# Optimization experiments

Hardware: AMD Instinct MI355X
Metric: run time of the kernel (lower is better)

The kernel has to match this reference:

```python
import jax, jax.numpy as jnp
import numpy as np

B, T, C, H, N_LAYER, LAYER_ID = 4, 2048, 1024, 16, 12, 6
N = C // H
Q = 256  # T % 256 == 0 -> chunk size used by the module


def setup_inputs():
    key = jax.random.key(0)
    ks = jax.random.split(key, 9)
    r0 = LAYER_ID / (N_LAYER - 1)
    r1 = 1.0 - LAYER_ID / N_LAYER
    ddd = (jnp.arange(C, dtype=jnp.float32) / C)[None, None, :]
    h = jnp.arange(C, dtype=jnp.float32)
    s = 1.0 / np.sqrt(C)
    return {
        "x": jax.random.normal(ks[0], (B, T, C), jnp.float32),
        "time_maa_x": 1.0 - ddd ** r1,
        "time_maa_w": 1.0 - ddd ** r1,
        "time_maa_k": 1.0 - ddd ** r1,
        "time_maa_v": 1.0 - (ddd ** r1 + 0.3 * r0),
        "time_maa_r": 1.0 - ddd ** (0.5 * r1),
        "maa_w1": jax.random.uniform(ks[1], (C, 4 * 32), jnp.float32, minval=-0.01, maxval=0.01),
        "maa_w2": jax.random.uniform(ks[2], (4, 32, C), jnp.float32, minval=-0.01, maxval=0.01),
        "decay_w1": jax.random.uniform(ks[3], (C, 64), jnp.float32, minval=-0.01, maxval=0.01),
        "decay_w2": jax.random.uniform(ks[4], (64, C), jnp.float32, minval=-0.01, maxval=0.01),
        "time_decay": (-6.0 + 5.0 * (h / (C - 1)) ** (0.7 + 1.3 * r0))[None, None, :],
        "time_faaaa": (r0 * (1.0 - h / (C - 1))).reshape(1, H, 1, 1, N),
        "Wr": jax.random.normal(ks[5], (C, C), jnp.float32) * s,
        "Wk": jax.random.normal(ks[6], (C, C), jnp.float32) * s,
        "Wv": jax.random.normal(ks[7], (C, C), jnp.float32) * s,
        "Wo": jax.random.normal(ks[8], (C, C), jnp.float32) * s,
        "ln_g": jnp.ones((C,), jnp.float32),
        "ln_b": jnp.zeros((C,), jnp.float32),
    }


def _forward(x, time_maa_x, time_maa_w, time_maa_k, time_maa_v, time_maa_r,
             maa_w1, maa_w2, decay_w1, decay_w2, time_decay, time_faaaa,
             Wr, Wk, Wv, Wo, ln_g, ln_b):
    b, t, c = x.shape
    nc = t // Q
    # time_shift: zero-pad one step at front of time axis, drop last step
    xx = jnp.pad(x, ((0, 0), (1, 0), (0, 0)))[:, :-1] - x
    xxx = x + xx * time_maa_x
    m = jnp.tanh(xxx @ maa_w1).reshape(b, t, 4, -1)  # [B,T,4,32]
    m = jnp.einsum('btfd,fdc->fbtc', m, maa_w2)       # [4,B,T,C]
    mw, mk, mv, mr = m[0], m[1], m[2], m[3]
    xw = x + xx * (time_maa_w + mw)
    xk = x + xx * (time_maa_k + mk)
    xv = x + xx * (time_maa_v + mv)
    xr = x + xx * (time_maa_r + mr)
    r = (xr @ Wr).reshape(b, t, H, N).transpose(0, 2, 1, 3)  # [B,H,T,N]
    k = (xk @ Wk).reshape(b, t, H, N).transpose(0, 2, 1, 3)
    v = (xv @ Wv).reshape(b, t, H, N).transpose(0, 2, 1, 3)
    w = time_decay + jnp.tanh(xw @ decay_w1) @ decay_w2      # [B,T,C]
    w = w.reshape(b, t, H, N).transpose(0, 2, 1, 3).mean(axis=-1)  # [B,H,T]
    w_log = -jnp.exp(w)
    wc = w_log.reshape(b, H, nc, Q, 1)
    wc_cum = jnp.cumsum(wc, axis=-2)
    shifted = jnp.pad(wc_cum, ((0, 0), (0, 0), (0, 0), (1, 0), (0, 0)))[..., :-1, :]
    ws_log = wc.sum(axis=-2, keepdims=True)   # [B,H,nc,1,1]
    w_inter = jnp.exp(ws_log - wc_cum)        # [B,H,nc,Q,1]
    w_intra = jnp.exp(wc_cum - wc)            # [B,H,nc,Q,1]
    ws = jnp.exp(ws_log)                      # [B,H,nc,1,1]
    A = shifted - jnp.swapaxes(wc_cum, -1, -2)  # [B,H,nc,Q,Q]
    strict = jnp.tril(jnp.ones((Q, Q), dtype=bool), -1)
    # torch: tril() -> exp() -> tril(-1)  ==  exp on strict-lower, zero elsewhere
    w_mask = jnp.where(strict, jnp.exp(jnp.where(strict, A, 0.0)), 0.0)
    rr = r.reshape(b, H, nc, Q, N)
    kk = k.reshape(b, H, nc, Q, N)
    vv = v.reshape(b, H, nc, Q, N)
    kv = jnp.einsum('bhcqn,bhcqm->bhcnm', kk * w_inter, vv)  # [B,H,nc,N,N]

    def step(state, inp):
        ws_i, kv_i = inp
        return ws_i * state + kv_i, state  # emit state BEFORE update (as in torch loop)

    _, states = jax.lax.scan(step, jnp.zeros((b, H, N, N), x.dtype),
                             (jnp.moveaxis(ws, 2, 0), jnp.moveaxis(kv, 2, 0)))
    states = jnp.moveaxis(states, 0, 2)  # [B,H,nc,N,N]
    inter = jnp.einsum('bhcqn,bhcnm->bhcqm', rr * w_intra, states)
    scores = jnp.einsum('bhcqn,bhckn->bhcqk', rr, kk) * w_mask
    diag = jnp.sum(rr * (time_faaaa * kk), axis=-1)  # [B,H,nc,Q]
    intra = jnp.einsum('bhcqk,bhckm->bhcqm', scores, vv) + diag[..., None] * vv
    y = (inter + intra).reshape(b, H, t, N).transpose(0, 2, 1, 3).reshape(b, t, c)
    mu = y.mean(axis=-1, keepdims=True)
    var = ((y - mu) ** 2).mean(axis=-1, keepdims=True)
    y = (y - mu) / jnp.sqrt(var + 1e-5) * ln_g + ln_b  # ln_x
    return y @ Wo  # output projection (dropout p=0)


def reference(x, time_maa_x, time_maa_w, time_maa_k, time_maa_v, time_maa_r,
              maa_w1, maa_w2, decay_w1, decay_w2, time_decay, time_faaaa,
              Wr, Wk, Wv, Wo, ln_g, ln_b):
    return _forward(x, time_maa_x, time_maa_w, time_maa_k, time_maa_v, time_maa_r,
                    maa_w1, maa_w2, decay_w1, decay_w2, time_decay, time_faaaa,
                    Wr, Wk, Wv, Wo, ln_g, ln_b)
```

## Files before the change

### kernel.cpp

```cpp
#include <hip/hip_runtime.h>
#include <math.h>

#define BB 4
#define TT 2048
#define CC 1024
#define HH 16
#define NN 64
#define QQ 256
#define NCH 8
#define BT 8192

typedef unsigned short u16;
typedef __attribute__((ext_vector_type(8))) short bf16x8;
typedef __attribute__((ext_vector_type(4))) short bf16x4;
typedef __attribute__((ext_vector_type(4))) float f32x4;
typedef __attribute__((ext_vector_type(4))) u16 u16x4;

__device__ inline u16 f2b(float x) {
  union { float f; unsigned u; } v;
  v.f = x;
  unsigned r = v.u + 0x7FFFu + ((v.u >> 16) & 1u);
  return (u16)(r >> 16);
}
__device__ inline float b2f(u16 u) {
  union { unsigned u; float f; } v;
  v.u = ((unsigned)u) << 16;
  return v.f;
}
__device__ inline bf16x8 ldfrag(const u16* p) {
  bf16x4 lo = *(const bf16x4*)p;
  bf16x4 hi = *(const bf16x4*)(p + 4);
  return __builtin_shufflevector(lo, hi, 0, 1, 2, 3, 4, 5, 6, 7);
}
__device__ inline void stage_tile(const u16* __restrict__ g, size_t base,
                                  int pitch, int tid, u16* __restrict__ lds) {
#pragma unroll
  for (int it = 0; it < 2; it++) {
    int cidx = tid + it * 256;
    int r = cidx >> 3, c8 = (cidx & 7) * 8;
    bf16x8 v = *(const bf16x8*)(g + base + (size_t)r * pitch + c8);
    *(bf16x4*)(lds + r * 72 + c8) = __builtin_shufflevector(v, v, 0, 1, 2, 3);
    *(bf16x4*)(lds + r * 72 + c8 + 4) = __builtin_shufflevector(v, v, 4, 5, 6, 7);
  }
}

__global__ __launch_bounds__(256) void mix_kernel(const float* __restrict__ x,
                                                  const float* __restrict__ tmx,
                                                  u16* __restrict__ xxxb) {
  size_t e = ((size_t)blockIdx.x * 256 + threadIdx.x) * 4;
  int c = (int)(e & 1023);
  size_t row = e >> 10;
  int t = (int)(row & 2047);
  float4 xv = *(const float4*)(x + e);
  float4 pv = make_float4(0.f, 0.f, 0.f, 0.f);
  if (t > 0) pv = *(const float4*)(x + e - 1024);
  float4 d = make_float4(pv.x - xv.x, pv.y - xv.y, pv.z - xv.z, pv.w - xv.w);
  u16x4 o;
  o.x = f2b(xv.x + d.x * tmx[c + 0]);
  o.y = f2b(xv.y + d.y * tmx[c + 1]);
  o.z = f2b(xv.z + d.z * tmx[c + 2]);
  o.w = f2b(xv.w + d.w * tmx[c + 3]);
  *(u16x4*)(xxxb + e) = o;
}

__global__ __launch_bounds__(256) void cvt_wT(const float* __restrict__ W0,
                                              const float* __restrict__ W1,
                                              const float* __restrict__ W2,
                                              const float* __restrict__ W3,
                                              u16* __restrict__ O0,
                                              u16* __restrict__ O1,
                                              u16* __restrict__ O2,
                                              u16* __restrict__ O3) {
  const float* W;
  u16* O;
  switch (blockIdx.z) {
    case 0: W = W0; O = O0; break;
    case 1: W = W1; O = O1; break;
    case 2: W = W2; O = O2; break;
    default: W = W3; O = O3; break;
  }
  __shared__ float t[64][65];
  int bx = blockIdx.x * 64;
  int by = blockIdx.y * 64;
#pragma unroll
  for (int it = 0; it < 16; it++) {
    int idx = it * 256 + threadIdx.x;
    int r = idx >> 6, c = idx & 63;
    t[r][c] = W[(size_t)(by + r) * 1024 + bx + c];
  }
  __syncthreads();
#pragma unroll
  for (int it = 0; it < 16; it++) {
    int idx = it * 256 + threadIdx.x;
    int n = idx >> 6, k = idx & 63;
    O[(size_t)(bx + n) * 1024 + by + k] = f2b(t[k][n]);
  }
}

__global__ __launch_bounds__(256) void cvt3_T(const float* __restrict__ w1,
                                              const float* __restrict__ w2,
                                              const float* __restrict__ d1,
                                              u16* __restrict__ o1,
                                              u16* __restrict__ o2,
                                              u16* __restrict__ o3,
                                              const float* __restrict__ dw2,
                                              const float* __restrict__ td,
                                              float* __restrict__ dw2r,
                                              float* __restrict__ tdr,
                                              u16* __restrict__ dw2rbT) {
  if (blockIdx.z == 3) {
    if (blockIdx.y != 0 || blockIdx.x >= 4) return;
    int idx = blockIdx.x * 256 + threadIdx.x;
    if (idx < 1024) {
      int j = idx >> 4, h = idx & 15;
      float s = 0.f;
      for (int n = 0; n < 64; n++) s += dw2[(size_t)j * 1024 + h * 64 + n];
      float m = s * (1.f / 64.f);
      dw2r[j * 16 + h] = m;
      dw2rbT[h * 64 + j] = f2b(m);
    }
    if (idx < 16) {
      float s = 0.f;
      for (int n = 0; n < 64; n++) s += td[idx * 64 + n];
      tdr[idx] = s * (1.f / 64.f);
    }
    return;
  }
  const float* in;
  u16* out;
  int R, C;
  switch (blockIdx.z) {
    case 0: in = w1; out = o1; R = 1024; C = 128; break;
    case 1: in = w2; out = o2; R = 128; C = 1024; break;
    default: in = d1; out = o3; R = 1024; C = 64; break;
  }
  int c0 = blockIdx.x * 64, r0 = blockIdx.y * 64;
  if (c0 >= C || r0 >= R) return;
  __shared__ float t[64][65];
#pragma unroll
  for (int it = 0; it < 16; it++) {
    int idx = it * 256 + threadIdx.x;
    int r = idx >> 6, c = idx & 63;
    t[r][c] = in[(size_t)(r0 + r) * C + c0 + c];
  }
  __syncthreads();
#pragma unroll
  for (int it = 0; it < 16; it++) {
    int idx = it * 256 + threadIdx.x;
    int c = idx >> 6, r = idx & 63;
    out[(size_t)(c0 + c) * R + r0 + r] = f2b(t[r][c]);
  }
}

__global__ __launch_bounds__(256) void gemm_maa(const u16* __restrict__ A,
                                                const u16* __restrict__ Bt,
                                                u16* __restrict__ Cb) {
  __shared__ u16 As[64 * 32];
  __shared__ u16 Bs[64 * 32];
  const int tid = threadIdx.x;
  const int lane = tid & 63;
  const int wave = tid >> 6;
  const int wc = wave * 16;
  const int fr = lane & 15;
  const int fq = lane >> 4;
  const int row0 = blockIdx.y * 64;
  const int col0 = blockIdx.x * 64;

  f32x4 acc[4];
#pragma unroll
  for (int i = 0; i < 4; i++) acc[i] = (f32x4){0.f, 0.f, 0.f, 0.f};

  const int ra = tid >> 2, ca = (tid & 3) * 8;

  for (int k0 = 0; k0 < 1024; k0 += 32) {
    __builtin_amdgcn_global_load_lds(
        (const __attribute__((address_space(1))) void*)(A + (size_t)(row0 + ra) * 1024 + k0 + ca),
        (__attribute__((address_space(3))) void*)(As + tid * 8), 16, 0, 0);
    __builtin_amdgcn_global_load_lds(
        (const __attribute__((address_space(1))) void*)(Bt + (size_t)(col0 + ra) * 1024 + k0 + ca),
        (__attribute__((address_space(3))) void*)(Bs + tid * 8), 16, 0, 0);
    __syncthreads();
    bf16x8 bf = *(const bf16x8*)(Bs + ((wc + fr) * 32 + fq * 8));
#pragma unroll
    for (int i = 0; i < 4; i++) {
      bf16x8 af = *(const bf16x8*)(As + ((i * 16 + fr) * 32 + fq * 8));
      acc[i] = __builtin_amdgcn_mfma_f32_16x16x32_bf16(af, bf, acc[i], 0, 0, 0);
    }
    __syncthreads();
  }
#pragma unroll
  for (int i = 0; i < 4; i++) {
    int grow = row0 + i * 16 + fq * 4;
#pragma unroll
    for (int r = 0; r < 4; r++)
      Cb[(size_t)(grow + r) * 128 + col0 + wc + fr] = f2b(tanhf(acc[i][r]));
  }
}

#define DP_ABUF 8192
#define DP_BBUF 16384
#define DP_SBUF 24576
#define DP_SMEM_BYTES 147456

template <bool TRIPLE, bool F32OUT>
__global__ __launch_bounds__(512, 2) void gemm_dp(
    const u16* __restrict__ A0, const u16* __restrict__ A1,
    const u16* __restrict__ A2, const u16* __restrict__ B0,
    const u16* __restrict__ B1, const u16* __restrict__ B2,
    float* __restrict__ Cf, u16* __restrict__ C0, u16* __restrict__ C1,
    u16* __restrict__ C2) {
  extern __shared__ __align__(16) u16 smem[];
  const int nwg = (int)(gridDim.x * gridDim.y * gridDim.z);
  const int wg = (int)(blockIdx.x + (blockIdx.y << 2) + (blockIdx.z << 8));
  const int cpx = nwg >> 3;
  const int swz = (wg & 7) * cpx + (wg >> 3);
  const int bx = swz & 3;
  const int by = (swz >> 2) & 63;
  const int bz = swz >> 8;

  const u16* __restrict__ A;
  const u16* __restrict__ Bt;
  u16* __restrict__ Cb;
  if (TRIPLE) {
    switch (bz) {
      case 0: A = A0; Bt = B0; Cb = C0; break;
      case 1: A = A1; Bt = B1; Cb = C1; break;
      default: A = A2; Bt = B2; Cb = C2; break;
    }
  } else {
    A = A0; Bt = B0; Cb = C0;
  }

  const int tid = threadIdx.x;
  const int lane = tid & 63;
  const int wave = tid >> 6;
  const int wr = (wave >> 2) * 64;
  const int wc = (wave & 3) * 64;
  const int fr = lane & 15;
  const int fq = lane >> 4;
  const int s8 = fr & 7;
  const int row0 = by * 128;
  const int col0 = bx * 256;

  int aoff[4][2], boff[4][2];
#pragma unroll
  for (int mi = 0; mi < 4; mi++)
#pragma unroll
    for (int ks = 0; ks < 2; ks++)
      aoff[mi][ks] = (wr + mi * 16 + fr) * 64 + (((ks * 4 + fq) ^ s8) * 8);
#pragma unroll
  for (int nj = 0; nj < 4; nj++)
#pragma unroll
    for (int ks = 0; ks < 2; ks++)
      boff[nj][ks] = (wc + nj * 16 + fr) * 64 + (((ks * 4 + fq) ^ s8) * 8);

  auto stage = [&](int kt, int q) {
    const u16* __restrict__ gA = A + (size_t)row0 * 1024 + kt * 64;
    const u16* __restrict__ gB = Bt + (size_t)col0 * 1024 + kt * 64;
    u16* dA = smem + q * DP_SBUF;
    u16* dB = dA + DP_ABUF;
#pragma unroll
    for (int p = 0; p < 2; p++) {
      int pos = tid + p * 512;
      int r = pos >> 3, gch = (pos & 7) ^ (r & 7);
      __builtin_amdgcn_global_load_lds(
          (const __attribute__((address_space(1))) void*)(gA + (size_t)r * 1024 + gch * 8),
          (__attribute__((address_space(3))) void*)(dA + pos * 8), 16, 0, 0);
    }
#pragma unroll
    for (int p = 0; p < 4; p++) {
      int pos = tid + p * 512;
      int r = pos >> 3, gch = (pos & 7) ^ (r & 7);
      __builtin_amdgcn_global_load_lds(
          (const __attribute__((address_space(1))) void*)(gB + (size_t)r * 1024 + gch * 8),
          (__attribute__((address_space(3))) void*)(dB + pos * 8), 16, 0, 0);
    }
  };

  f32x4 acc[4][4];
#pragma unroll
  for (int mi = 0; mi < 4; mi++)
#pragma unroll
    for (int nj = 0; nj < 4; nj++) acc[mi][nj] = (f32x4){0.f, 0.f, 0.f, 0.f};

  auto iter_body = [&](int qc, int qs, bool dostage, int t2) {
    if (dostage) stage(t2, qs);
    const u16* sA = smem + qc * DP_SBUF;
    const u16* sB = sA + DP_ABUF;
    bf16x8 av[4][2], bv[4][2];
#pragma unroll
    for (int mi = 0; mi < 4; mi++)
#pragma unroll
      for (int ks = 0; ks < 2; ks++)
        av[mi][ks] = *(const bf16x8*)(sA + aoff[mi][ks]);
#pragma unroll
    for (int nj = 0; nj < 4; nj++)
#pragma unroll
      for (int ks = 0; ks < 2; ks++)
        bv[nj][ks] = *(const bf16x8*)(sB + boff[nj][ks]);
    __builtin_amdgcn_s_setprio(1);
#pragma unroll
    for (int ks = 0; ks < 2; ks++)
#pragma unroll
      for (int mi = 0; mi < 4; mi++)
#pragma unroll
        for (int nj = 0; nj < 4; nj++)
          acc[mi][nj] = __builtin_amdgcn_mfma_f32_16x16x32_bf16(
              av[mi][ks], bv[nj][ks], acc[mi][nj], 0, 0, 0);
    __builtin_amdgcn_s_setprio(0);
  };

  stage(0, 0);
  stage(1, 1);
  int qc = 0, qs = 2;
  for (int t = 0; t < 14; t++) {
    asm volatile("s_waitcnt vmcnt(6)" ::: "memory");
    __builtin_amdgcn_s_barrier();
    iter_body(qc, qs, true, t + 2);
    qc = (qc == 2) ? 0 : qc + 1;
    qs = (qs == 2) ? 0 : qs + 1;
  }
  asm volatile("s_waitcnt vmcnt(6)" ::: "memory");
  __builtin_amdgcn_s_barrier();
  iter_body(qc, 0, false, 0);
  qc = (qc == 2) ? 0 : qc + 1;
  asm volatile("s_waitcnt vmcnt(0)" ::: "memory");
  __builtin_amdgcn_s_barrier();
  iter_body(qc, 0, false, 0);

#pragma unroll
  for (int mi = 0; mi < 4; mi++) {
    int grow = row0 + wr + mi * 16 + fq * 4;
#pragma unroll
    for (int nj = 0; nj < 4; nj++) {
      int gcol = col0 + wc + nj * 16 + fr;
#pragma unroll
      for (int r = 0; r < 4; r++) {
        if (F32OUT)
          Cf[(size_t)(grow + r) * 1024 + gcol] = acc[mi][nj][r];
        else
          Cb[(size_t)(grow + r) * 1024 + gcol] = f2b(acc[mi][nj][r]);
      }
    }
  }
}

__global__ __launch_bounds__(256) void blend_mfma(
    const u16* __restrict__ mb, const u16* __restrict__ w2T,
    const float* __restrict__ x,
    const float* __restrict__ tmw, const float* __restrict__ tmk,
    const float* __restrict__ tmv, const float* __restrict__ tmr,
    u16* __restrict__ xwb, u16* __restrict__ xkb, u16* __restrict__ xvb,
    u16* __restrict__ xrb) {
  __shared__ u16 mS[64 * 136];
  __shared__ u16 wS[64 * 136];
  const int tid = threadIdx.x;
  const int lane = tid & 63;
  const int w = tid >> 6;
  const int fr = lane & 15;
  const int fq = lane >> 4;
  const int c0 = blockIdx.x * 64;
  const int bt0 = blockIdx.y * 64;

#pragma unroll
  for (int it = 0; it < 4; it++) {
    int idx = tid + it * 256;
    int r = idx >> 4, c8 = (idx & 15) * 8;
    bf16x8 v = *(const bf16x8*)(mb + (size_t)(bt0 + r) * 128 + c8);
    *(bf16x4*)(mS + r * 136 + c8) = __builtin_shufflevector(v, v, 0, 1, 2, 3);
    *(bf16x4*)(mS + r * 136 + c8 + 4) = __builtin_shufflevector(v, v, 4, 5, 6, 7);
    bf16x8 u = *(const bf16x8*)(w2T + (size_t)(c0 + r) * 128 + c8);
    *(bf16x4*)(wS + r * 136 + c8) = __builtin_shufflevector(u, u, 0, 1, 2, 3);
    *(bf16x4*)(wS + r * 136 + c8 + 4) = __builtin_shufflevector(u, u, 4, 5, 6, 7);
  }
  __syncthreads();

  f32x4 acc[4][4];
#pragma unroll
  for (int j = 0; j < 4; j++)
#pragma unroll
    for (int f = 0; f < 4; f++) acc[j][f] = (f32x4){0.f, 0.f, 0.f, 0.f};

#pragma unroll
  for (int f = 0; f < 4; f++) {
    bf16x8 aA = ldfrag(mS + (w * 16 + fr) * 136 + f * 32 + fq * 8);
#pragma unroll
    for (int j = 0; j < 4; j++) {
      bf16x8 bB = ldfrag(wS + (j * 16 + fr) * 136 + f * 32 + fq * 8);
      acc[j][f] = __builtin_amdgcn_mfma_f32_16x16x32_bf16(aA, bB, acc[j][f], 0, 0, 0);
    }
  }

#pragma unroll
  for (int j = 0; j < 4; j++) {
    int c = c0 + j * 16 + fr;
    float w_ = tmw[c], k_ = tmk[c], v_ = tmv[c], r_ = tmr[c];
#pragma unroll
    for (int rr = 0; rr < 4; rr++) {
      int bt = bt0 + w * 16 + fq * 4 + rr;
      size_t g = (size_t)bt * 1024 + c;
      float xv_ = x[g];
      float xp = ((bt & 2047) != 0) ? x[g - 1024] : 0.f;
      float dx = xp - xv_;
      xwb[g] = f2b(xv_ + dx * (w_ + acc[j][0][rr]));
      xkb[g] = f2b(xv_ + dx * (k_ + acc[j][1][rr]));
      xvb[g] = f2b(xv_ + dx * (v_ + acc[j][2][rr]));
      xrb[g] = f2b(xv_ + dx * (r_ + acc[j][3][rr]));
    }
  }
}

__global__ __launch_bounds__(256) void decay_mfma(const u16* __restrict__ xwb,
                                                  const u16* __restrict__ d1T,
                                                  const u16* __restrict__ dw2rbT,
                                                  const float* __restrict__ tdr,
                                                  float* __restrict__ wlog) {
  __shared__ u16 As[32 * 64];
  __shared__ u16 Bs[64 * 64];
  __shared__ u16 h1S[32 * 72];
  __shared__ u16 dwS[16 * 72];
  const int tid = threadIdx.x;
  const int lane = tid & 63;
  const int w = tid >> 6;
  const int fr = lane & 15;
  const int fq = lane >> 4;
  const int s8 = fr & 7;
  const int bt0 = blockIdx.x * 32;

#pragma unroll
  for (int it = 0; it < 4; it++) {
    int idx = tid + it * 256;
    int r = idx >> 6, c = idx & 63;
    dwS[r * 72 + c] = dw2rbT[r * 64 + c];
  }

  f32x4 acc[2];
#pragma unroll
  for (int mi = 0; mi < 2; mi++) acc[mi] = (f32x4){0.f, 0.f, 0.f, 0.f};

  const int raA = tid >> 3;
  const int gchA = (tid & 7) ^ (raA & 7);

  for (int k0 = 0; k0 < 1024; k0 += 64) {
    __builtin_amdgcn_global_load_lds(
        (const __attribute__((address_space(1))) void*)(
            xwb + (size_t)(bt0 + raA) * 1024 + k0 + gchA * 8),
        (__attribute__((address_space(3))) void*)(As + tid * 8), 16, 0, 0);
#pragma unroll
    for (int p = 0; p < 2; p++) {
      int pos = tid + p * 256;
      int r = pos >> 3, gch = (pos & 7) ^ (r & 7);
      __builtin_amdgcn_global_load_lds(
          (const __attribute__((address_space(1))) void*)(
              d1T + (size_t)r * 1024 + k0 + gch * 8),
          (__attribute__((address_space(3))) void*)(Bs + pos * 8), 16, 0, 0);
    }
    __syncthreads();
#pragma unroll
    for (int ks = 0; ks < 2; ks++) {
      int chunk = ((ks * 4 + fq) ^ s8) * 8;
      bf16x8 bB = *(const bf16x8*)(Bs + (w * 16 + fr) * 64 + chunk);
#pragma unroll
      for (int mi = 0; mi < 2; mi++) {
        bf16x8 aA = *(const bf16x8*)(As + (mi * 16 + fr) * 64 + chunk);
        acc[mi] = __builtin_amdgcn_mfma_f32_16x16x32_bf16(aA, bB, acc[mi], 0, 0, 0);
      }
    }
    __syncthreads();
  }
#pragma unroll
  for (int mi = 0; mi < 2; mi++)
#pragma unroll
    for (int rr = 0; rr < 4; rr++)
      h1S[(mi * 16 + fq * 4 + rr) * 72 + w * 16 + fr] = f2b(tanhf(acc[mi][rr]));
  __syncthreads();

  if (w < 2) {
    f32x4 a2 = (f32x4){0.f, 0.f, 0.f, 0.f};
#pragma unroll
    for (int ks = 0; ks < 2; ks++) {
      bf16x8 aA = ldfrag(h1S + (w * 16 + fr) * 72 + ks * 32 + fq * 8);
      bf16x8 bB = ldfrag(dwS + fr * 72 + ks * 32 + fq * 8);
      a2 = __builtin_amdgcn_mfma_f32_16x16x32_bf16(aA, bB, a2, 0, 0, 0);
    }
    float tdv = tdr[fr];
#pragma unroll
    for (int rr = 0; rr < 4; rr++) {
      int bt = bt0 + w * 16 + fq * 4 + rr;
      int b = bt >> 11, tl = bt & 2047;
      wlog[((size_t)(b * 16 + fr)) * 2048 + tl] = -__expf(tdv + a2[rr]);
    }
  }
}

__global__ __launch_bounds__(256) void wprep_kernel(const float* __restrict__ wlog,
                                                    float* __restrict__ cum,
                                                    float* __restrict__ excl,
                                                    float* __restrict__ wsl) {
  int bid = blockIdx.x;
  int c = bid & 7, bh = bid >> 3;
  int q = threadIdx.x;
  float v = wlog[(size_t)bh * 2048 + c * 256 + q];
  __shared__ float s[256];
  s[q] = v;
  float val = v;
  for (int off = 1; off < 256; off <<= 1) {
    __syncthreads();
    float t = (q >= off) ? s[q - off] : 0.f;
    __syncthreads();
    val += t;
    s[q] = val;
  }
  __syncthreads();
  float total = s[255];
  cum[(size_t)bid * 256 + q] = val;
  excl[(size_t)bid * 256 + q] = val - v;
  if (q == 0) wsl[bid] = total;
}

__global__ __launch_bounds__(256) void kvfuse_kernel(
    const u16* __restrict__ vb, const u16* __restrict__ kb,
    const u16* __restrict__ rb, const float* __restrict__ faaaa,
    const float* __restrict__ cum, const float* __restrict__ wsl,
    u16* __restrict__ vT, float* __restrict__ diagG, float* __restrict__ kvb) {
  int bid = blockIdx.x;
  int c = bid & 7, bh = bid >> 3;
  int b = bh >> 4, h = bh & 15;
  __shared__ float tv[64][65];
  __shared__ float tk[64][65];
  __shared__ u16 kSb[64 * 72];
  __shared__ u16 vSb[64 * 72];
  __shared__ float wfacS[256];
  __shared__ float faS[64];
  const int tid = threadIdx.x;
  const int lane = tid & 63;
  const int w = tid >> 6;
  const int fr = lane & 15;
  const int fq = lane >> 4;
  const int m = lane;

  float wslog = wsl[bid];
  wfacS[tid] = __expf(wslog - cum[(size_t)bid * 256 + tid]);
  if (tid < 64) faS[tid] = faaaa[h * 64 + tid];

  f32x4 acc[4];
#pragma unroll
  for (int j = 0; j < 4; j++) acc[j] = (f32x4){0.f, 0.f, 0.f, 0.f};

  for (int qt = 0; qt < 4; qt++) {
    __syncthreads();
    float fam = faS[m];
    int t0 = c * QQ + qt * 64;
#pragma unroll
    for (int it = 0; it < 16; it++) {
      int r = it * 4 + w;
      size_t g = ((size_t)(b * TT + t0 + r)) * CC + h * 64 + m;
      float vraw = b2f(vb[g]);
      float kraw = b2f(kb[g]);
      float rraw = b2f(rb[g]);
      tv[r][m] = vraw;
      tk[r][m] = kraw;
      float s = rraw * fam * kraw;
      s += __shfl_xor(s, 1);
      s += __shfl_xor(s, 2);
      s += __shfl_xor(s, 4);
      s += __shfl_xor(s, 8);
      s += __shfl_xor(s, 16);
      s += __shfl_xor(s, 32);
      if (m == 0) diagG[(size_t)bh * 2048 + t0 + r] = s;
    }
    __syncthreads();
#pragma unroll
    for (int it = 0; it < 16; it++) {
      int idx = it * 256 + tid;
      int mm = idx >> 6, tl = idx & 63;
      float vv = tv[tl][mm];
      float kk = tk[tl][mm] * wfacS[qt * 64 + tl];
      u16 vbv = f2b(vv);
      vT[((size_t)(bh * 64 + mm)) * TT + t0 + tl] = vbv;
      vSb[mm * 72 + tl] = vbv;
      kSb[mm * 72 + tl] = f2b(kk);
    }
    __syncthreads();
#pragma unroll
    for (int ks = 0; ks < 2; ks++) {
      bf16x8 aA = ldfrag(kSb + (w * 16 + fr) * 72 + ks * 32 + fq * 8);
#pragma unroll
      for (int j = 0; j < 4; j++) {
        bf16x8 bB = ldfrag(vSb + (j * 16 + fr) * 72 + ks * 32 + fq * 8);
        acc[j] = __builtin_amdgcn_mfma_f32_16x16x32_bf16(aA, bB, acc[j], 0, 0, 0);
      }
    }
  }
#pragma unroll
  for (int j = 0; j < 4; j++)
#pragma unroll
    for (int rr = 0; rr < 4; rr++)
      kvb[(size_t)bid * 4096 + (w * 16 + fq * 4 + rr) * 64 + j * 16 + fr] = acc[j][rr];
}

__global__ __launch_bounds__(256) void scan_kernel(const float* __restrict__ kvb,
                                                   const float* __restrict__ wsl,
                                                   float* __restrict__ st) {
  int bh = blockIdx.x >> 2;
  int sl = blockIdx.x & 3;
  int tid = threadIdx.x;
  f32x4 s = (f32x4){0.f, 0.f, 0.f, 0.f};
  for (int c = 0; c < 8; c++) {
    int bid = bh * 8 + c;
    float w = __expf(wsl[bid]);
    size_t e = (size_t)bid * 4096 + sl * 1024 + tid * 4;
    f32x4 kv = *(const f32x4*)(kvb + e);
    *(f32x4*)(st + e) = s;
    s = w * s + kv;
  }
}

__global__ __launch_bounds__(256) void attn_mfma(
    const u16* __restrict__ rb, const u16* __restrict__ kb,
    const u16* __restrict__ vT, const float* __restrict__ stg,
    const float* __restrict__ cum, const float* __restrict__ excl,
    const float* __restrict__ diagG, float* __restrict__ y) {
  int bid = blockIdx.x;
  int c = bid & 7, bh = bid >> 3;
  int b = bh >> 4, h = bh & 15;
  __shared__ u16 rt[64 * 72];
  __shared__ u16 kt[64 * 72];
  __shared__ u16 vt[64 * 72];
  __shared__ u16 pt[64 * 72];
  __shared__ u16 stT[64 * 72];
  __shared__ float cumS[256], exS[256], diagS[256], ekS[256];

  const int tid = threadIdx.x;
  const int lane = tid & 63;
  const int w = tid >> 6;
  const int fr = lane & 15;
  const int fq = lane >> 4;

  cumS[tid] = cum[(size_t)bid * 256 + tid];
  exS[tid] = excl[(size_t)bid * 256 + tid];
  diagS[tid] = diagG[(size_t)bh * 2048 + c * 256 + tid];
#pragma unroll
  for (int it = 0; it < 16; it++) {
    int idx = tid + it * 256;
    int n = idx >> 6, mm = idx & 63;
    stT[mm * 72 + n] = f2b(stg[(size_t)bid * 4096 + idx]);
  }
  __syncthreads();
  const float ccm = cumS[127];
  ekS[tid] = __expf(ccm - cumS[tid]);

  const size_t rowbase = ((size_t)b * TT + c * QQ) * CC + h * 64;
  const size_t vbase0 = (size_t)bh * 64 * TT + c * QQ;

  for (int qt = 0; qt < 4; qt++) {
    __syncthreads();
    stage_tile(rb, rowbase + (size_t)(qt * 64) * CC, CC, tid, rt);
    __syncthreads();

    f32x4 acc[4];
#pragma unroll
    for (int jm = 0; jm < 4; jm++) acc[jm] = (f32x4){0.f, 0.f, 0.f, 0.f};
    bf16x8 rA[2];
    rA[0] = ldfrag(rt + (w * 16 + fr) * 72 + fq * 8);
    rA[1] = ldfrag(rt + (w * 16 + fr) * 72 + 32 + fq * 8);
#pragma unroll
    for (int ks = 0; ks < 2; ks++)
#pragma unroll
      for (int jm = 0; jm < 4; jm++) {
        bf16x8 bB = ldfrag(stT + (jm * 16 + fr) * 72 + ks * 32 + fq * 8);
        acc[jm] = __builtin_amdgcn_mfma_f32_16x16x32_bf16(rA[ks], bB, acc[jm], 0, 0, 0);
      }
    int ql0 = w * 16 + fq * 4;
    float er[4], eqc[4];
#pragma unroll
    for (int rr = 0; rr < 4; rr++) {
      float ex = exS[qt * 64 + ql0 + rr];
      er[rr] = __expf(ex);
      eqc[rr] = __expf(ex - ccm);
    }
#pragma unroll
    for (int jm = 0; jm < 4; jm++)
#pragma unroll
      for (int rr = 0; rr < 4; rr++) acc[jm][rr] *= er[rr];

    for (int kti = 0; kti <= qt; kti++) {
      __syncthreads();
      stage_tile(kb, rowbase + (size_t)(kti * 64) * CC, CC, tid, kt);
      stage_tile(vT, vbase0 + (size_t)(kti * 64), TT, tid, vt);
      __syncthreads();

      f32x4 sacc[4];
#pragma unroll
      for (int jj = 0; jj < 4; jj++) sacc[jj] = (f32x4){0.f, 0.f, 0.f, 0.f};
#pragma unroll
      for (int ks = 0; ks < 2; ks++)
#pragma unroll
        for (int jj = 0; jj < 4; jj++) {
          bf16x8 bB = ldfrag(kt + (jj * 16 + fr) * 72 + ks * 32 + fq * 8);
          sacc[jj] = __builtin_amdgcn_mfma_f32_16x16x32_bf16(rA[ks], bB, sacc[jj], 0, 0, 0);
        }
#pragma unroll
      for (int jj = 0; jj < 4; jj++) {
        int kcol = kti * 64 + jj * 16 + fr;
        float ek = ekS[kcol];
#pragma unroll
        for (int rr = 0; rr < 4; rr++) {
          int qrow = qt * 64 + ql0 + rr;
          float vsc;
          if (kcol < qrow)
            vsc = sacc[jj][rr] * eqc[rr] * ek;
          else if (kcol == qrow)
            vsc = diagS[qrow];
          else
            vsc = 0.f;
          pt[(ql0 + rr) * 72 + jj * 16 + fr] = f2b(vsc);
        }
      }
      __syncthreads();
#pragma unroll
      for (int ks = 0; ks < 2; ks++) {
        bf16x8 pA = ldfrag(pt + (w * 16 + fr) * 72 + ks * 32 + fq * 8);
#pragma unroll
        for (int jm = 0; jm < 4; jm++) {
          bf16x8 vB = ldfrag(vt + (jm * 16 + fr) * 72 + ks * 32 + fq * 8);
          acc[jm] = __builtin_amdgcn_mfma_f32_16x16x32_bf16(pA, vB, acc[jm], 0, 0, 0);
        }
      }
    }
    int qg0 = qt * 64 + w * 16 + fq * 4;
#pragma unroll
    for (int jm = 0; jm < 4; jm++)
#pragma unroll
      for (int rr = 0; rr < 4; rr++)
        y[rowbase + (size_t)(qg0 + rr) * CC + jm * 16 + fr] = acc[jm][rr];
  }
}

__global__ __launch_bounds__(256) void ln_kernel(const float* __restrict__ y,
                                                 const float* __restrict__ g,
                                                 const float* __restrict__ bta,
                                                 u16* __restrict__ out) {
  __shared__ float red[8];
  int bt = blockIdx.x;
  int tid = threadIdx.x;
  float4 v = *(const float4*)(y + (size_t)bt * 1024 + tid * 4);
  float s = v.x + v.y + v.z + v.w;
#pragma unroll
  for (int off = 32; off > 0; off >>= 1) s += __shfl_down(s, off);
  if ((tid & 63) == 0) red[tid >> 6] = s;
  __syncthreads();
  if (tid == 0) red[4] = red[0] + red[1] + red[2] + red[3];
  __syncthreads();
  float mu = red[4] * (1.f / 1024.f);
  float d0 = v.x - mu, d1 = v.y - mu, d2 = v.z - mu, d3 = v.w - mu;
  float s2 = d0 * d0 + d1 * d1 + d2 * d2 + d3 * d3;
#pragma unroll
  for (int off = 32; off > 0; off >>= 1) s2 += __shfl_down(s2, off);
  __syncthreads();
  if ((tid & 63) == 0) red[tid >> 6] = s2;
  __syncthreads();
  if (tid == 0) red[5] = red[0] + red[1] + red[2] + red[3];
  __syncthreads();
  float var = red[5] * (1.f / 1024.f);
  float rstd = rsqrtf(var + 1e-5f);
  float4 g4 = *(const float4*)(g + tid * 4);
  float4 b4 = *(const float4*)(bta + tid * 4);
  u16x4 o;
  o.x = f2b(d0 * rstd * g4.x + b4.x);
  o.y = f2b(d1 * rstd * g4.y + b4.y);
  o.z = f2b(d2 * rstd * g4.z + b4.z);
  o.w = f2b(d3 * rstd * g4.w + b4.w);
  *(u16x4*)(out + (size_t)bt * 1024 + tid * 4) = o;
}

extern "C" void kernel_launch(void* const* d_in, const int* in_sizes, int n_in,
                              void* d_out, int out_size, void* d_ws,
                              size_t ws_size, hipStream_t stream) {
  const float* x = (const float*)d_in[0];
  const float* tmx = (const float*)d_in[1];
  const float* tmw = (const float*)d_in[2];
  const float* tmk = (const float*)d_in[3];
  const float* tmv = (const float*)d_in[4];
  const float* tmr = (const float*)d_in[5];
  const float* maa_w1 = (const float*)d_in[6];
  const float* maa_w2 = (const float*)d_in[7];
  const float* decay_w1 = (const float*)d_in[8];
  const float* decay_w2 = (const float*)d_in[9];
  const float* time_decay = (const float*)d_in[10];
  const float* faaaa = (const float*)d_in[11];
  const float* Wr = (const float*)d_in[12];
  const float* Wk = (const float*)d_in[13];
  const float* Wv = (const float*)d_in[14];
  const float* Wo = (const float*)d_in[15];
  const float* lng = (const float*)d_in[16];
  const float* lnb = (const float*)d_in[17];
  float* out = (float*)d_out;
  float* ws = (float*)d_ws;

  const size_t S = (size_t)BT * CC;

  float* y_ = ws;
  float* dw2r = ws + S;
  float* tdr = dw2r + 1024;
  float* wlog = tdr + 1024;
  float* cum = wlog + 131072;
  float* excl = cum + 131072;
  float* wsl = excl + 131072;
  float* diagG = wsl + 1024;
  float* kvb = diagG + 131072;
  float* stb = kvb + (size_t)512 * 4096;
  float* fend = stb + (size_t)512 * 4096;
  u16* xxxb = (u16*)fend;
  u16* mb = xxxb + S;
  u16* xkb = mb + (size_t)BT * 128;
  u16* xvb = xkb + S;
  u16* xrb = xvb + S;
  u16* xwb = xrb + S;
  u16* rb16 = xwb + S;
  u16* kb16 = rb16 + S;
  u16* Vb = kb16 + S;
  u16* Wrt = Vb + S;
  u16* Wkt = Wrt + (size_t)1024 * 1024;
  u16* Wvt = Wkt + (size_t)1024 * 1024;
  u16* Wot = Wvt + (size_t)1024 * 1024;
  u16* w1T = Wot + (size_t)1024 * 1024;
  u16* w2T = w1T + (size_t)128 * 1024;
  u16* d1T = w2T + (size_t)1024 * 128;
  u16* dw2rbT = d1T + (size_t)64 * 1024;
  u16* vT = xxxb;
  u16* ylnb = xkb;

  static bool attr_done = false;
  if (!attr_done) {
    hipFuncSetAttribute((const void*)gemm_dp<true, false>,
                        hipFuncAttributeMaxDynamicSharedMemorySize, DP_SMEM_BYTES);
    hipFuncSetAttribute((const void*)gemm_dp<false, true>,
                        hipFuncAttributeMaxDynamicSharedMemorySize, DP_SMEM_BYTES);
    attr_done = true;
  }

  cvt_wT<<<dim3(16, 16, 4), 256, 0, stream>>>(Wr, Wk, Wv, Wo, Wrt, Wkt, Wvt, Wot);
  cvt3_T<<<dim3(16, 16, 4), 256, 0, stream>>>(maa_w1, maa_w2, decay_w1, w1T,
                                              w2T, d1T, decay_w2, time_decay,
                                              dw2r, tdr, dw2rbT);
  mix_kernel<<<8192, 256, 0, stream>>>(x, tmx, xxxb);
  gemm_maa<<<dim3(2, 128), 256, 0, stream>>>(xxxb, w1T, mb);
  blend_mfma<<<dim3(16, 128), 256, 0, stream>>>(mb, w2T, x, tmw, tmk, tmv, tmr,
                                                xwb, xkb, xvb, xrb);
  decay_mfma<<<256, 256, 0, stream>>>(xwb, d1T, dw2rbT, tdr, wlog);
  wprep_kernel<<<512, 256, 0, stream>>>(wlog, cum, excl, wsl);
  gemm_dp<true, false><<<dim3(4, 64, 3), 512, DP_SMEM_BYTES, stream>>>(
      xrb, xkb, xvb, Wrt, Wkt, Wvt, nullptr, rb16, kb16, Vb);
  kvfuse_kernel<<<512, 256, 0, stream>>>(Vb, kb16, rb16, faaaa, cum, wsl, vT,
                                         diagG, kvb);
  scan_kernel<<<256, 256, 0, stream>>>(kvb, wsl, stb);
  attn_mfma<<<512, 256, 0, stream>>>(rb16, kb16, vT, stb, cum, excl, diagG, y_);
  ln_kernel<<<BT, 256, 0, stream>>>(y_, lng, lnb, ylnb);
  gemm_dp<false, true><<<dim3(4, 64, 1), 512, DP_SMEM_BYTES, stream>>>(
      ylnb, nullptr, nullptr, Wot, nullptr, nullptr, out, nullptr, nullptr,
      nullptr);
}
```

Before: 349.4 us.

## Pair query tiles in attention kernel and merge weight conversion launches

The attention kernel now processes two 64-row query tiles per pass, so each staged K/V tile is reused by both query tiles. This roughly halves K/V staging traffic and the barriers around it. In exchange it keeps twice as many accumulators live, adds extra barriers inside the inner loop, and reuses the score buffer to hold the second query tile, which raises register pressure. Separately, the two weight-transpose/convert kernels are merged into one launch to save a kernel launch.

```diff
diff --git a/kernel.cpp b/kernel.cpp
--- a/kernel.cpp
+++ b/kernel.cpp
@@ -63,52 +63,18 @@
   *(u16x4*)(xxxb + e) = o;
 }
 
-__global__ __launch_bounds__(256) void cvt_wT(const float* __restrict__ W0,
-                                              const float* __restrict__ W1,
-                                              const float* __restrict__ W2,
-                                              const float* __restrict__ W3,
-                                              u16* __restrict__ O0,
-                                              u16* __restrict__ O1,
-                                              u16* __restrict__ O2,
-                                              u16* __restrict__ O3) {
-  const float* W;
-  u16* O;
-  switch (blockIdx.z) {
-    case 0: W = W0; O = O0; break;
-    case 1: W = W1; O = O1; break;
-    case 2: W = W2; O = O2; break;
-    default: W = W3; O = O3; break;
-  }
-  __shared__ float t[64][65];
-  int bx = blockIdx.x * 64;
-  int by = blockIdx.y * 64;
-#pragma unroll
-  for (int it = 0; it < 16; it++) {
-    int idx = it * 256 + threadIdx.x;
-    int r = idx >> 6, c = idx & 63;
-    t[r][c] = W[(size_t)(by + r) * 1024 + bx + c];
-  }
-  __syncthreads();
-#pragma unroll
-  for (int it = 0; it < 16; it++) {
-    int idx = it * 256 + threadIdx.x;
-    int n = idx >> 6, k = idx & 63;
-    O[(size_t)(bx + n) * 1024 + by + k] = f2b(t[k][n]);
-  }
-}
-
-__global__ __launch_bounds__(256) void cvt3_T(const float* __restrict__ w1,
-                                              const float* __restrict__ w2,
-                                              const float* __restrict__ d1,
-                                              u16* __restrict__ o1,
-                                              u16* __restrict__ o2,
-                                              u16* __restrict__ o3,
-                                              const float* __restrict__ dw2,
-                                              const float* __restrict__ td,
-                                              float* __restrict__ dw2r,
-                                              float* __restrict__ tdr,
-                                              u16* __restrict__ dw2rbT) {
-  if (blockIdx.z == 3) {
+__global__ __launch_bounds__(256) void cvt_all(
+    const float* __restrict__ W0, const float* __restrict__ W1,
+    const float* __restrict__ W2, const float* __restrict__ W3,
+    u16* __restrict__ O0, u16* __restrict__ O1, u16* __restrict__ O2,
+    u16* __restrict__ O3, const float* __restrict__ w1,
+    const float* __restrict__ w2, const float* __restrict__ d1,
+    u16* __restrict__ o1, u16* __restrict__ o2, u16* __restrict__ o3,
+    const float* __restrict__ dw2, const float* __restrict__ td,
+    float* __restrict__ dw2r, float* __restrict__ tdr,
+    u16* __restrict__ dw2rbT) {
+  int z = blockIdx.z;
+  if (z == 7) {
     if (blockIdx.y != 0 || blockIdx.x >= 4) return;
     int idx = blockIdx.x * 256 + threadIdx.x;
     if (idx < 1024) {
@@ -129,9 +95,13 @@
   const float* in;
   u16* out;
   int R, C;
-  switch (blockIdx.z) {
-    case 0: in = w1; out = o1; R = 1024; C = 128; break;
-    case 1: in = w2; out = o2; R = 128; C = 1024; break;
+  switch (z) {
+    case 0: in = W0; out = O0; R = 1024; C = 1024; break;
+    case 1: in = W1; out = O1; R = 1024; C = 1024; break;
+    case 2: in = W2; out = O2; R = 1024; C = 1024; break;
+    case 3: in = W3; out = O3; R = 1024; C = 1024; break;
+    case 4: in = w1; out = o1; R = 1024; C = 128; break;
+    case 5: in = w2; out = o2; R = 128; C = 1024; break;
     default: in = d1; out = o3; R = 1024; C = 64; break;
   }
   int c0 = blockIdx.x * 64, r0 = blockIdx.y * 64;
@@ -652,88 +622,109 @@
 
   const size_t rowbase = ((size_t)b * TT + c * QQ) * CC + h * 64;
   const size_t vbase0 = (size_t)bh * 64 * TT + c * QQ;
-
-  for (int qt = 0; qt < 4; qt++) {
-    __syncthreads();
-    stage_tile(rb, rowbase + (size_t)(qt * 64) * CC, CC, tid, rt);
-    __syncthreads();
-
-    f32x4 acc[4];
-#pragma unroll
-    for (int jm = 0; jm < 4; jm++) acc[jm] = (f32x4){0.f, 0.f, 0.f, 0.f};
-    bf16x8 rA[2];
-    rA[0] = ldfrag(rt + (w * 16 + fr) * 72 + fq * 8);
-    rA[1] = ldfrag(rt + (w * 16 + fr) * 72 + 32 + fq * 8);
-#pragma unroll
-    for (int ks = 0; ks < 2; ks++)
-#pragma unroll
-      for (int jm = 0; jm < 4; jm++) {
-        bf16x8 bB = ldfrag(stT + (jm * 16 + fr) * 72 + ks * 32 + fq * 8);
-        acc[jm] = __builtin_amdgcn_mfma_f32_16x16x32_bf16(rA[ks], bB, acc[jm], 0, 0, 0);
+  const int ql0 = w * 16 + fq * 4;
+
+#pragma unroll
+  for (int p = 0; p < 2; p++) {
+    __syncthreads();
+    stage_tile(rb, rowbase + (size_t)((2 * p) * 64) * CC, CC, tid, rt);
+    stage_tile(rb, rowbase + (size_t)((2 * p + 1) * 64) * CC, CC, tid, pt);
+    __syncthreads();
+    bf16x8 rA[2][2];
+    rA[0][0] = ldfrag(rt + (w * 16 + fr) * 72 + fq * 8);
+    rA[0][1] = ldfrag(rt + (w * 16 + fr) * 72 + 32 + fq * 8);
+    rA[1][0] = ldfrag(pt + (w * 16 + fr) * 72 + fq * 8);
+    rA[1][1] = ldfrag(pt + (w * 16 + fr) * 72 + 32 + fq * 8);
+
+    f32x4 acc[2][4];
+    float eqc[2][4];
+#pragma unroll
+    for (int j = 0; j < 2; j++) {
+      int qt = 2 * p + j;
+#pragma unroll
+      for (int jm = 0; jm < 4; jm++) acc[j][jm] = (f32x4){0.f, 0.f, 0.f, 0.f};
+#pragma unroll
+      for (int ks = 0; ks < 2; ks++)
+#pragma unroll
+        for (int jm = 0; jm < 4; jm++) {
+          bf16x8 bB = ldfrag(stT + (jm * 16 + fr) * 72 + ks * 32 + fq * 8);
+          acc[j][jm] = __builtin_amdgcn_mfma_f32_16x16x32_bf16(
+              rA[j][ks], bB, acc[j][jm], 0, 0, 0);
+        }
+      float er[4];
+#pragma unroll
+      for (int rr = 0; rr < 4; rr++) {
+        float ex = exS[qt * 64 + ql0 + rr];
+        er[rr] = __expf(ex);
+        eqc[j][rr] = __expf(ex - ccm);
       }
-    int ql0 = w * 16 + fq * 4;
-    float er[4], eqc[4];
-#pragma unroll
-    for (int rr = 0; rr < 4; rr++) {
-      float ex = exS[qt * 64 + ql0 + rr];
-      er[rr] = __expf(ex);
-      eqc[rr] = __expf(ex - ccm);
-    }
-#pragma unroll
-    for (int jm = 0; jm < 4; jm++)
-#pragma unroll
-      for (int rr = 0; rr < 4; rr++) acc[jm][rr] *= er[rr];
-
-    for (int kti = 0; kti <= qt; kti++) {
+#pragma unroll
+      for (int jm = 0; jm < 4; jm++)
+#pragma unroll
+        for (int rr = 0; rr < 4; rr++) acc[j][jm][rr] *= er[rr];
+    }
+
+#pragma unroll
+    for (int kti = 0; kti < 2 * p + 2; kti++) {
       __syncthreads();
       stage_tile(kb, rowbase + (size_t)(kti * 64) * CC, CC, tid, kt);
       stage_tile(vT, vbase0 + (size_t)(kti * 64), TT, tid, vt);
       __syncthreads();
-
-      f32x4 sacc[4];
-#pragma unroll
-      for (int jj = 0; jj < 4; jj++) sacc[jj] = (f32x4){0.f, 0.f, 0.f, 0.f};
-#pragma unroll
-      for (int ks = 0; ks < 2; ks++)
+#pragma unroll
+      for (int j = 0; j < 2; j++) {
+        int qt = 2 * p + j;
+        if (kti > qt) continue;
+        f32x4 sacc[4];
+#pragma unroll
+        for (int jj = 0; jj < 4; jj++) sacc[jj] = (f32x4){0.f, 0.f, 0.f, 0.f};
+#pragma unroll
+        for (int ks = 0; ks < 2; ks++)
+#pragma unroll
+          for (int jj = 0; jj < 4; jj++) {
+            bf16x8 bB = ldfrag(kt + (jj * 16 + fr) * 72 + ks * 32 + fq * 8);
+            sacc[jj] = __builtin_amdgcn_mfma_f32_16x16x32_bf16(
+                rA[j][ks], bB, sacc[jj], 0, 0, 0);
+          }
 #pragma unroll
         for (int jj = 0; jj < 4; jj++) {
-          bf16x8 bB = ldfrag(kt + (jj * 16 + fr) * 72 + ks * 32 + fq * 8);
-          sacc[jj] = __builtin_amdgcn_mfma_f32_16x16x32_bf16(rA[ks], bB, sacc[jj], 0, 0, 0);
+          int kcol = kti * 64 + jj * 16 + fr;
+          float ek = ekS[kcol];
+#pragma unroll
+          for (int rr = 0; rr < 4; rr++) {
+            int qrow = qt * 64 + ql0 + rr;
+            float vsc;
+            if (kcol < qrow)
+              vsc = sacc[jj][rr] * eqc[j][rr] * ek;
+            else if (kcol == qrow)
+              vsc = diagS[qrow];
+            else
+              vsc = 0.f;
+            pt[(ql0 + rr) * 72 + jj * 16 + fr] = f2b(vsc);
+          }
         }
-#pragma unroll
-      for (int jj = 0; jj < 4; jj++) {
-        int kcol = kti * 64 + jj * 16 + fr;
-        float ek = ekS[kcol];
-#pragma unroll
-        for (int rr = 0; rr < 4; rr++) {
-          int qrow = qt * 64 + ql0 + rr;
-          float vsc;
-          if (kcol < qrow)
-            vsc = sacc[jj][rr] * eqc[rr] * ek;
-          else if (kcol == qrow)
-            vsc = diagS[qrow];
-          else
-            vsc = 0.f;
-          pt[(ql0 + rr) * 72 + jj * 16 + fr] = f2b(vsc);
+        __syncthreads();
+#pragma unroll
+        for (int ks = 0; ks < 2; ks++) {
+          bf16x8 pA = ldfrag(pt + (w * 16 + fr) * 72 + ks * 32 + fq * 8);
+#pragma unroll
+          for (int jm = 0; jm < 4; jm++) {
+            bf16x8 vB = ldfrag(vt + (jm * 16 + fr) * 72 + ks * 32 + fq * 8);
+            acc[j][jm] = __builtin_amdgcn_mfma_f32_16x16x32_bf16(
+                pA, vB, acc[j][jm], 0, 0, 0);
+          }
         }
+        __syncthreads();
       }
-      __syncthreads();
-#pragma unroll
-      for (int ks = 0; ks < 2; ks++) {
-        bf16x8 pA = ldfrag(pt + (w * 16 + fr) * 72 + ks * 32 + fq * 8);
-#pragma unroll
-        for (int jm = 0; jm < 4; jm++) {
-          bf16x8 vB = ldfrag(vt + (jm * 16 + fr) * 72 + ks * 32 + fq * 8);
-          acc[jm] = __builtin_amdgcn_mfma_f32_16x16x32_bf16(pA, vB, acc[jm], 0, 0, 0);
-        }
-      }
-    }
-    int qg0 = qt * 64 + w * 16 + fq * 4;
-#pragma unroll
-    for (int jm = 0; jm < 4; jm++)
-#pragma unroll
-      for (int rr = 0; rr < 4; rr++)
-        y[rowbase + (size_t)(qg0 + rr) * CC + jm * 16 + fr] = acc[jm][rr];
+    }
+#pragma unroll
+    for (int j = 0; j < 2; j++) {
+      int qg0 = (2 * p + j) * 64 + ql0;
+#pragma unroll
+      for (int jm = 0; jm < 4; jm++)
+#pragma unroll
+        for (int rr = 0; rr < 4; rr++)
+          y[rowbase + (size_t)(qg0 + rr) * CC + jm * 16 + fr] = acc[j][jm][rr];
+    }
   }
 }
 
@@ -840,10 +831,9 @@
     attr_done = true;
   }
 
-  cvt_wT<<<dim3(16, 16, 4), 256, 0, stream>>>(Wr, Wk, Wv, Wo, Wrt, Wkt, Wvt, Wot);
-  cvt3_T<<<dim3(16, 16, 4), 256, 0, stream>>>(maa_w1, maa_w2, decay_w1, w1T,
-                                              w2T, d1T, decay_w2, time_decay,
-                                              dw2r, tdr, dw2rbT);
+  cvt_all<<<dim3(16, 16, 8), 256, 0, stream>>>(
+      Wr, Wk, Wv, Wo, Wrt, Wkt, Wvt, Wot, maa_w1, maa_w2, decay_w1, w1T, w2T,
+      d1T, decay_w2, time_decay, dw2r, tdr, dw2rbT);
   mix_kernel<<<8192, 256, 0, stream>>>(x, tmx, xxxb);
   gemm_maa<<<dim3(2, 128), 256, 0, stream>>>(xxxb, w1T, mb);
   blend_mfma<<<dim3(16, 128), 256, 0, stream>>>(mb, w2T, x, tmw, tmk, tmv, tmr,
```

Result: no change. 347.8 us (-0.5%).
